# Kernel tuning notes

Measured on AMD Instinct MI355X. Metric: run time of the kernel, lower is better.

Reference implementation:

```python
import jax, jax.numpy as jnp
import numpy as np

# ---- config (YOLOv4-style, TRAIN_SIZE=608, P2..P5) ----
STRIDES = (4.0, 8.0, 16.0, 32.0)
ANCHORS = np.array([
    [[12, 16], [19, 36], [40, 28], [36, 75]],
    [[36, 75], [76, 55], [72, 146], [142, 110]],
    [[72, 146], [142, 110], [192, 243], [459, 401]],
    [[142, 110], [192, 243], [300, 300], [459, 401]],
], dtype=np.float32)  # [LEVELS, NUM_ANCHORS, 2]
MAX_PROP = 100
SCORE_THRESH = 0.25
IOU_THRESH = 0.5


def decode_prediction(p, anchors, stride):
    # p: [b, A, h, w, 6] -> [b, A*h*w, 5] with xyxy + score
    b, A, h, w, _ = p.shape
    txy, twh, conf, cls = p[..., :2], p[..., 2:4], p[..., 4:5], p[..., 5:6]
    gx, gy = jnp.meshgrid(jnp.arange(w, dtype=p.dtype), jnp.arange(h, dtype=p.dtype))
    grid = jnp.stack([gx, gy], axis=-1)[None, None]  # [1,1,h,w,2]
    xy = (jax.nn.sigmoid(txy) + grid) * stride
    wh = jnp.exp(twh) * anchors[None, :, None, None, :]
    score = jax.nn.sigmoid(conf) * jax.nn.sigmoid(cls)
    x1y1 = xy - 0.5 * wh
    x2y2 = xy + 0.5 * wh
    out = jnp.concatenate([x1y1, x2y2, score], axis=-1)  # [b,A,h,w,5]
    return out.reshape(b, A * h * w, 5)


def _iou_one_vs_all(box, boxes):
    # box: [4], boxes: [N,4] (xyxy)
    lt = jnp.maximum(box[:2], boxes[:, :2])
    rb = jnp.minimum(box[2:], boxes[:, 2:])
    wh = jnp.maximum(rb - lt, 0.0)
    inter = wh[:, 0] * wh[:, 1]
    a1 = jnp.maximum(box[2] - box[0], 0.0) * jnp.maximum(box[3] - box[1], 0.0)
    a2 = jnp.maximum(boxes[:, 2] - boxes[:, 0], 0.0) * jnp.maximum(boxes[:, 3] - boxes[:, 1], 0.0)
    return inter / (a1 + a2 - inter + 1e-9)


def _nms_single(boxes, scores):
    # greedy NMS, padded to MAX_PROP with zero rows
    s0 = jnp.where(scores >= SCORE_THRESH, scores, 0.0)

    def step(s, _):
        i = jnp.argmax(s)
        sc = s[i]
        box = boxes[i]
        keep = sc > 0.0
        row = jnp.where(keep, jnp.concatenate([box, sc[None]]), jnp.zeros(5, boxes.dtype))
        iou = _iou_one_vs_all(box, boxes)
        s = jnp.where((iou > IOU_THRESH) & keep, 0.0, s)
        s = s.at[i].set(0.0)
        return s, row

    _, props = jax.lax.scan(step, s0, None, length=MAX_PROP)
    return props  # [MAX_PROP, 5]


def entry_stop_gradients(t, mask):
    # gradient flows only through entries where mask==1
    return jax.lax.stop_gradient(t) * (1.0 - mask) + t * mask


def _forward(p2, p3, p4, p5):
    anchors = jnp.asarray(ANCHORS)
    d2 = decode_prediction(p2, anchors[0], STRIDES[0])
    d3 = decode_prediction(p3, anchors[1], STRIDES[1])
    d4 = decode_prediction(p4, anchors[2], STRIDES[2])
    d5 = decode_prediction(p5, anchors[3], STRIDES[3])
    proposals = jnp.concatenate([d2, d3, d4, d5], axis=1)  # [b, N, 5]
    proposals = jax.vmap(lambda pr: _nms_single(pr[:, :4], pr[:, 4]))(proposals)  # [b, MAX_PROP, 5]
    mask = (jnp.sum(proposals[..., :4], axis=-1) != 0.0).astype(proposals.dtype)[..., None]
    return entry_stop_gradients(proposals, mask)


def setup_inputs() -> dict:
    key = jax.random.key(0)
    k2, k3, k4, k5 = jax.random.split(key, 4)
    b, A, ch = 32, 4, 6
    return {
        "p2": jax.random.normal(k2, (b, A, 152, 152, ch), dtype=jnp.float32),
        "p3": jax.random.normal(k3, (b, A, 76, 76, ch), dtype=jnp.float32),
        "p4": jax.random.normal(k4, (b, A, 38, 38, ch), dtype=jnp.float32),
        "p5": jax.random.normal(k5, (b, A, 19, 19, ch), dtype=jnp.float32),
    }


def reference(p2, p3, p4, p5):
    return _forward(p2, p3, p4, p5)
```

## Files before the change

### kernel.cpp

```cpp
#include <hip/hip_runtime.h>
#include <cstdint>
#include <cstddef>

typedef unsigned int u32;
typedef unsigned long long u64;

#define NTOT 122740
#define NPAIR 61370
#define KTOP 1024
#define WIN  256
#define NBIN 4096
#define SCORE_T 0.25f
#define TBITS 0x3E800000u
#define HSPLIT_BITS 0x3EFFF000u
#define CSTRIDE 64
#define CAP_H 40960
#define CAP_L 20480


#define WS_CANDH 8192
#define WS_CANDL 10493952

__device__ __forceinline__ float sigm(float x) { return 1.0f / (1.0f + expf(-x)); }

__device__ __forceinline__ int score_bin(u32 bits) {
  return min(4095, 1 + (int)((bits - TBITS) >> 12));
}

__device__ __forceinline__ u64 shfl_u64(u64 x, int src) {
  int lo = __shfl((int)(u32)x, src, 64);
  int hi = __shfl((int)(u32)(x >> 32), src, 64);
  return ((u64)(u32)hi << 32) | (u32)lo;
}

__device__ __forceinline__ void score_pair(int P, int b,
    const float* __restrict__ p2, const float* __restrict__ p3,
    const float* __restrict__ p4, const float* __restrict__ p5,
    u32& b0, u32& b1, u32& gi0, u32& gi1)
{
  int t0 = 2 * P;
  const float* p; int l0, LN;
  if (t0 < 92416)       { p = p2; l0 = t0;          LN = 92416; }
  else if (t0 < 115520) { p = p3; l0 = t0 - 92416;  LN = 23104; }
  else if (t0 < 121296) { p = p4; l0 = t0 - 115520; LN = 5776;  }
  else                  { p = p5; l0 = t0 - 121296; LN = 1444;  }
  const float* q = p + ((size_t)b * LN + (size_t)l0) * 6;
  float4 v1 = *(const float4*)(q + 4);
  float4 v2 = *(const float4*)(q + 8);
  float s0 = sigm(v1.x) * sigm(v1.y);
  float s1 = sigm(v2.z) * sigm(v2.w);
  b0 = (s0 >= SCORE_T) ? __float_as_uint(s0) : 0u;
  b1 = (s1 >= SCORE_T) ? __float_as_uint(s1) : 0u;
  gi0 = (u32)t0; gi1 = (u32)(t0 + 1);
}

__device__ float4 decode_box_from_gidx(u32 gidx, int b,
    const float* __restrict__ p2, const float* __restrict__ p3,
    const float* __restrict__ p4, const float* __restrict__ p5)
{
  const float* p; int t, H, W; float stride;
  float aw0, ah0, aw1, ah1, aw2, ah2, aw3, ah3;
  if (gidx < 92416u) {
    p = p2 + (size_t)b * 92416 * 6; t = (int)gidx; H = 152; W = 152; stride = 4.0f;
    aw0=12.f; ah0=16.f; aw1=19.f; ah1=36.f; aw2=40.f; ah2=28.f; aw3=36.f; ah3=75.f;
  } else if (gidx < 115520u) {
    p = p3 + (size_t)b * 23104 * 6; t = (int)(gidx - 92416u); H = 76; W = 76; stride = 8.0f;
    aw0=36.f; ah0=75.f; aw1=76.f; ah1=55.f; aw2=72.f; ah2=146.f; aw3=142.f; ah3=110.f;
  } else if (gidx < 121296u) {
    p = p4 + (size_t)b * 5776 * 6; t = (int)(gidx - 115520u); H = 38; W = 38; stride = 16.0f;
    aw0=72.f; ah0=146.f; aw1=142.f; ah1=110.f; aw2=192.f; ah2=243.f; aw3=459.f; ah3=401.f;
  } else {
    p = p5 + (size_t)b * 1444 * 6; t = (int)(gidx - 121296u); H = 19; W = 19; stride = 32.0f;
    aw0=142.f; ah0=110.f; aw1=192.f; ah1=243.f; aw2=300.f; ah2=300.f; aw3=459.f; ah3=401.f;
  }
  int HW = H * W;
  int a = t / HW;
  int r = t - a * HW;
  int y = r / W;
  int x = r - y * W;
  const float* q = p + (size_t)t * 6;
  float2 t01 = *(const float2*)(q + 0);
  float2 t23 = *(const float2*)(q + 2);
  float cx = (sigm(t01.x) + (float)x) * stride;
  float cy = (sigm(t01.y) + (float)y) * stride;
  float aw = (a == 0) ? aw0 : (a == 1) ? aw1 : (a == 2) ? aw2 : aw3;
  float ah = (a == 0) ? ah0 : (a == 1) ? ah1 : (a == 2) ? ah2 : ah3;
  float bw = expf(t23.x) * aw;
  float bh = expf(t23.y) * ah;
  return make_float4(cx - 0.5f * bw, cy - 0.5f * bh, cx + 0.5f * bw, cy + 0.5f * bh);
}

__device__ __forceinline__ bool iou_gt(float4 A, float4 B) {
  float ltx = fmaxf(A.x, B.x), lty = fmaxf(A.y, B.y);
  float rbx = fminf(A.z, B.z), rby = fminf(A.w, B.w);
  float w = fmaxf(rbx - ltx, 0.0f), h = fmaxf(rby - lty, 0.0f);
  float inter = w * h;
  float a1 = fmaxf(A.z - A.x, 0.0f) * fmaxf(A.w - A.y, 0.0f);
  float a2 = fmaxf(B.z - B.x, 0.0f) * fmaxf(B.w - B.y, 0.0f);
  float iou = inter / (a1 + a2 - inter + 1e-9f);
  return iou > 0.5f;
}

__global__ __launch_bounds__(256)
void decode_kernel(const float* __restrict__ p2, const float* __restrict__ p3,
                   const float* __restrict__ p4, const float* __restrict__ p5,
                   u32* __restrict__ counters,
                   uint2* __restrict__ candH, uint2* __restrict__ candL)
{
  __shared__ uint2 stH[1024];
  __shared__ uint2 stL[1024];
  __shared__ u32 s_cH, s_cL, s_bH, s_bL;
  const int tid = threadIdx.x;
  const int b = blockIdx.y;
  if (tid == 0) { s_cH = 0u; s_cL = 0u; }
  __syncthreads();

  const int pbase = blockIdx.x * 512;
  #pragma unroll
  for (int k = 0; k < 2; ++k) {
    int P = pbase + k * 256 + tid;
    if (P < NPAIR) {
      u32 b0, b1, gi0, gi1;
      score_pair(P, b, p2, p3, p4, p5, b0, b1, gi0, gi1);
      if (b0) {
        bool H = (b0 >= HSPLIT_BITS);
        u32 pos = atomicAdd(H ? &s_cH : &s_cL, 1u);
        (H ? stH : stL)[pos] = make_uint2(b0, gi0);
      }
      if (b1) {
        bool H = (b1 >= HSPLIT_BITS);
        u32 pos = atomicAdd(H ? &s_cH : &s_cL, 1u);
        (H ? stH : stL)[pos] = make_uint2(b1, gi1);
      }
    }
  }
  __syncthreads();
  if (tid == 0) {
    if (s_cH) s_bH = atomicAdd(&counters[(size_t)b * CSTRIDE],     s_cH);
    if (s_cL) s_bL = atomicAdd(&counters[(size_t)b * CSTRIDE + 1], s_cL);
  }
  __syncthreads();
  uint2* gH = candH + (size_t)b * CAP_H;
  uint2* gL = candL + (size_t)b * CAP_L;
  const u32 mH = s_cH, mL = s_cL;
  for (u32 i = tid; i < mH; i += 256) { u32 d = s_bH + i; if (d < (u32)CAP_H) gH[d] = stH[i]; }
  for (u32 i = tid; i < mL; i += 256) { u32 d = s_bL + i; if (d < (u32)CAP_L) gL[d] = stL[i]; }
}

__global__ __launch_bounds__(1024, 1)
void mega_kernel(const u32* __restrict__ counters,
                 const uint2* __restrict__ candH, const uint2* __restrict__ candL,
                 const float* __restrict__ p2, const float* __restrict__ p3,
                 const float* __restrict__ p4, const float* __restrict__ p5,
                 float* __restrict__ out)
{
  const int b = blockIdx.x;
  const int tid = threadIdx.x;

  __shared__ u32 sstart[NBIN];
  __shared__ u32 scur[NBIN];
  __shared__ u64 skey[KTOP];
  __shared__ u64 skey2[KTOP];
  __shared__ float4 sbox[WIN];
  __shared__ u64 smat[WIN * 4];
  __shared__ float4 selbox[100];
  __shared__ int s_misc[4];
  __shared__ int s_B, s_n;

  const u32 nHc = counters[(size_t)b * CSTRIDE];
  const u32 nLc = counters[(size_t)b * CSTRIDE + 1];
  const bool readL = (nHc < (u32)KTOP);
  const bool fb = (nHc > (u32)CAP_H) || (readL && nLc > (u32)CAP_L);

  for (int i = tid; i < NBIN; i += 1024) scur[i] = 0u;
  for (int i = tid; i < KTOP; i += 1024) { skey[i] = 0ull; skey2[i] = 0ull; }
  __syncthreads();

  if (!fb) {
    const uint2* gH = candH + (size_t)b * CAP_H;
    for (u32 i = tid; i < nHc; i += 1024) atomicAdd(&scur[score_bin(gH[i].x)], 1u);
    if (readL) {
      const uint2* gL = candL + (size_t)b * CAP_L;
      for (u32 i = tid; i < nLc; i += 1024) atomicAdd(&scur[score_bin(gL[i].x)], 1u);
    }
  } else {
    for (int P = tid; P < NPAIR; P += 1024) {
      u32 b0, b1, gi0, gi1;
      score_pair(P, b, p2, p3, p4, p5, b0, b1, gi0, gi1);
      if (b0) atomicAdd(&scur[score_bin(b0)], 1u);
      if (b1) atomicAdd(&scur[score_bin(b1)], 1u);
    }
  }
  __syncthreads();

  if (tid < 64) {
    u32 h[64];
    #pragma unroll
    for (int k = 0; k < 64; ++k) h[k] = scur[tid * 64 + k];
    u32 lsum = 0;
    #pragma unroll
    for (int k = 0; k < 64; ++k) lsum += h[k];
    u32 S = lsum;
    #pragma unroll
    for (int off = 1; off < 64; off <<= 1) {
      u32 v = (u32)__shfl_down((int)S, off, 64);
      if (tid + off < 64) S += v;
    }
    u32 c = S - lsum;
    int Bv = -1; u32 nv = 0;
    for (int k = 63; k >= 0; --k) {
      sstart[tid * 64 + k] = c;
      c += h[k];
      if (c <= (u32)KTOP) { Bv = tid * 64 + k; nv = c; }
    }
    scur[tid]      = (Bv < 0) ? 0xFFFFFFFFu : (u32)Bv;
    scur[64 + tid] = nv;
  }
  __syncthreads();
  if (tid == 0) {
    u32 bb = 0xFFFFFFFFu, nn = 0;
    for (int l = 0; l < 64; ++l) {
      u32 v = scur[l];
      if (v < bb) { bb = v; nn = scur[64 + l]; }
    }
    if (bb == 0xFFFFFFFFu) { s_B = 4095; s_n = KTOP; }
    else { s_B = max((int)bb, 1); s_n = (int)nn; }
  }
  __syncthreads();
  const int B = s_B;
  const int n = min(s_n, KTOP);

  for (int i = tid; i < NBIN; i += 1024) scur[i] = sstart[i];
  __syncthreads();

  if (!fb) {
    const uint2* gH = candH + (size_t)b * CAP_H;
    for (u32 i = tid; i < nHc; i += 1024) {
      uint2 e = gH[i];
      int bin = score_bin(e.x);
      if (bin >= B) {
        u32 slot = atomicAdd(&scur[bin], 1u);
        if (slot < (u32)KTOP) skey[slot] = ((u64)e.x << 32) | (u32)(~e.y);
      }
    }
    if (readL) {
      const uint2* gL = candL + (size_t)b * CAP_L;
      for (u32 i = tid; i < nLc; i += 1024) {
        uint2 e = gL[i];
        int bin = score_bin(e.x);
        if (bin >= B) {
          u32 slot = atomicAdd(&scur[bin], 1u);
          if (slot < (u32)KTOP) skey[slot] = ((u64)e.x << 32) | (u32)(~e.y);
        }
      }
    }
  } else {
    for (int P = tid; P < NPAIR; P += 1024) {
      u32 b0, b1, gi0, gi1;
      score_pair(P, b, p2, p3, p4, p5, b0, b1, gi0, gi1);
      if (b0) { int bin = score_bin(b0);
        if (bin >= B) { u32 slot = atomicAdd(&scur[bin], 1u);
          if (slot < (u32)KTOP) skey[slot] = ((u64)b0 << 32) | (u32)(~gi0); } }
      if (b1) { int bin = score_bin(b1);
        if (bin >= B) { u32 slot = atomicAdd(&scur[bin], 1u);
          if (slot < (u32)KTOP) skey[slot] = ((u64)b1 << 32) | (u32)(~gi1); } }
    }
  }
  __syncthreads();

  for (int s = tid; s < n; s += 1024) {
    u64 k = skey[s];
    int bin = score_bin((u32)(k >> 32));
    int st = (int)sstart[bin];
    int en = (int)scur[bin];
    u32 r = 0;
    for (int j = st; j < en; ++j) r += (skey[j] > k) ? 1u : 0u;
    skey2[st + r] = k;
  }
  __syncthreads();

  const int Wn = min(n, WIN);

  if (tid < WIN) {
    sbox[tid] = (tid < Wn) ? decode_box_from_gidx(~(u32)skey2[tid], b, p2, p3, p4, p5)
                           : make_float4(0.f, 0.f, 0.f, 0.f);
  }
  __syncthreads();

  {
    int row = tid & 255, word = tid >> 8;
    u64 bits = 0;
    if (row < Wn) {
      float4 A = sbox[row];
      int j0 = word * 64;
      int je = min(64, Wn - j0);
      for (int j = 0; j < je; ++j)
        if (iou_gt(A, sbox[j0 + j])) bits |= (1ull << j);
    }
    smat[word * 256 + row] = bits;
  }
  __syncthreads();

  if (tid < 64) {
    const int lane = tid;
    u64 m0[4], m1[4], m2[4], m3[4];
    #pragma unroll
    for (int w = 0; w < 4; ++w) {
      m0[w] = smat[w * 256 +   0 + lane];
      m1[w] = smat[w * 256 +  64 + lane];
      m2[w] = smat[w * 256 + 128 + lane];
      m3[w] = smat[w * 256 + 192 + lane];
    }
    u64 live[4];
    #pragma unroll
    for (int g2 = 0; g2 < 4; ++g2) {
      int lo = g2 * 64;
      live[g2] = (Wn >= lo + 64) ? ~0ull : (Wn > lo ? ((1ull << (Wn - lo)) - 1ull) : 0ull);
    }
    int sel = 0;
    #pragma unroll 1
    for (int w2 = 0; w2 < 4; ++w2) {
      while (live[w2] && sel < 100) {
        int j = (int)__ffsll(live[w2]) - 1;
        int p = (w2 << 6) + j;
        u64 r0, r1, r2, r3;
        if (w2 == 0)      { r0 = shfl_u64(m0[0], j); r1 = shfl_u64(m0[1], j); r2 = shfl_u64(m0[2], j); r3 = shfl_u64(m0[3], j); }
        else if (w2 == 1) { r0 = shfl_u64(m1[0], j); r1 = shfl_u64(m1[1], j); r2 = shfl_u64(m1[2], j); r3 = shfl_u64(m1[3], j); }
        else if (w2 == 2) { r0 = shfl_u64(m2[0], j); r1 = shfl_u64(m2[1], j); r2 = shfl_u64(m2[2], j); r3 = shfl_u64(m2[3], j); }
        else              { r0 = shfl_u64(m3[0], j); r1 = shfl_u64(m3[1], j); r2 = shfl_u64(m3[2], j); r3 = shfl_u64(m3[3], j); }
        live[0] &= ~r0; live[1] &= ~r1; live[2] &= ~r2; live[3] &= ~r3;
        live[w2] &= ~(1ull << j);
        if (lane == 0) {
          float4 box = sbox[p];
          u64 k = skey2[p];
          float sc = __uint_as_float((u32)(k >> 32));
          selbox[sel] = box;
          float* orow = out + (size_t)b * 500 + (size_t)sel * 5;
          orow[0] = box.x; orow[1] = box.y; orow[2] = box.z; orow[3] = box.w; orow[4] = sc;
        }
        sel++;
      }
    }
    if (lane == 0) {
      s_misc[2] = sel;
      s_misc[3] = (sel < 100 && n > WIN) ? 1 : 0;
    }
  }
  __syncthreads();

  if (s_misc[3]) {
    if (tid < 64) {
      const int lane = tid;
      int sel = s_misc[2];
      for (int p = WIN; p < n && sel < 100; ++p) {
        u64 k = skey2[p];
        float4 box = decode_box_from_gidx(~(u32)k, b, p2, p3, p4, p5);
        bool hit = false;
        if (lane < sel) hit = iou_gt(selbox[lane], box);
        if (lane + 64 < sel) hit = hit || iou_gt(selbox[lane + 64], box);
        u64 anyhit = __ballot(hit);
        if (anyhit == 0ull) {
          if (lane == 0) {
            selbox[sel] = box;
            float sc = __uint_as_float((u32)(k >> 32));
            float* orow = out + (size_t)b * 500 + (size_t)sel * 5;
            orow[0] = box.x; orow[1] = box.y; orow[2] = box.z; orow[3] = box.w; orow[4] = sc;
          }
          sel++;
        }
      }
      if (lane == 0) s_misc[2] = sel;
    }
  }
  __syncthreads();

  const int nsel = s_misc[2];
  for (int i = tid; i < (100 - nsel) * 5; i += 1024)
    out[(size_t)b * 500 + (size_t)nsel * 5 + i] = 0.0f;
}

extern "C" void kernel_launch(void* const* d_in, const int* in_sizes, int n_in,
                              void* d_out, int out_size, void* d_ws, size_t ws_size,
                              hipStream_t stream) {
  const float* p2 = (const float*)d_in[0];
  const float* p3 = (const float*)d_in[1];
  const float* p4 = (const float*)d_in[2];
  const float* p5 = (const float*)d_in[3];
  float* out = (float*)d_out;

  unsigned char* w = (unsigned char*)d_ws;
  u32*   counters = (u32*)w;
  uint2* candH    = (uint2*)(w + WS_CANDH);
  uint2* candL    = (uint2*)(w + WS_CANDL);

  hipMemsetAsync(counters, 0, 32 * CSTRIDE * sizeof(u32), stream);
  decode_kernel<<<dim3(120, 32), 256, 0, stream>>>(p2, p3, p4, p5,
                                                   counters, candH, candL);
  mega_kernel<<<32, 1024, 0, stream>>>(counters, candH, candL,
                                       p2, p3, p4, p5, out);
}
```

Baseline: 171.0 us.

## Stage decode inputs through LDS with coalesced float4 loads and split mega kernel

The decode kernel now loads each block's slice of raw predictions as contiguous float4 into shared memory and reads only the two score channels per row. This replaces strided per-pair loads and doubles the grid to 240 blocks per image. The mega kernel is split into a sort kernel, which writes sorted keys to workspace, and a separate NMS kernel, freeing shared memory. The bin-selection reduction also moves from a serial thread-0 loop to a wave shuffle-min. The risks are the cost of an extra launch and a global round-trip for the sorted keys, and candidates are silently dropped if a block's staging buffer exceeds 512.

```diff
diff --git a/kernel.cpp b/kernel.cpp
--- a/kernel.cpp
+++ b/kernel.cpp
@@ -17,9 +17,14 @@
 #define CAP_H 40960
 #define CAP_L 20480
 
-
-#define WS_CANDH 8192
-#define WS_CANDL 10493952
+#define F4TOT 184110
+#define F4B3 138624
+#define F4B4 173280
+#define F4B5 181944
+
+#define WS_SORTED 8192
+#define WS_CANDH  270336
+#define WS_CANDL  10756096
 
 __device__ __forceinline__ float sigm(float x) { return 1.0f / (1.0f + expf(-x)); }
 
@@ -107,30 +112,48 @@
                    u32* __restrict__ counters,
                    uint2* __restrict__ candH, uint2* __restrict__ candL)
 {
-  __shared__ uint2 stH[1024];
-  __shared__ uint2 stL[1024];
+  __shared__ float4 sbuf4[768];
+  __shared__ uint2 stH[512];
+  __shared__ uint2 stL[512];
   __shared__ u32 s_cH, s_cL, s_bH, s_bL;
   const int tid = threadIdx.x;
   const int b = blockIdx.y;
   if (tid == 0) { s_cH = 0u; s_cL = 0u; }
-  __syncthreads();
-
-  const int pbase = blockIdx.x * 512;
+
+  const float4* q2 = (const float4*)p2;
+  const float4* q3 = (const float4*)p3;
+  const float4* q4 = (const float4*)p4;
+  const float4* q5 = (const float4*)p5;
+
+  const int f4base = blockIdx.x * 768;
+  #pragma unroll
+  for (int j = 0; j < 3; ++j) {
+    int idx4 = f4base + j * 256 + tid;
+    if (idx4 < F4TOT) {
+      const float4* src;
+      if (idx4 < F4B3)      src = q2 + (size_t)b * 138624 + idx4;
+      else if (idx4 < F4B4) src = q3 + (size_t)b * 34656  + (idx4 - F4B3);
+      else if (idx4 < F4B5) src = q4 + (size_t)b * 8664   + (idx4 - F4B4);
+      else                  src = q5 + (size_t)b * 2166   + (idx4 - F4B5);
+      sbuf4[j * 256 + tid] = *src;
+    }
+  }
+  __syncthreads();
+
+  const float* sbuf = (const float*)sbuf4;
+  const int rbase = blockIdx.x * 512;
   #pragma unroll
   for (int k = 0; k < 2; ++k) {
-    int P = pbase + k * 256 + tid;
-    if (P < NPAIR) {
-      u32 b0, b1, gi0, gi1;
-      score_pair(P, b, p2, p3, p4, p5, b0, b1, gi0, gi1);
-      if (b0) {
-        bool H = (b0 >= HSPLIT_BITS);
+    int lr = 2 * tid + k;
+    int rg = rbase + lr;
+    if (rg < NTOT) {
+      float2 cc = *(const float2*)&sbuf[lr * 6 + 4];
+      float s = sigm(cc.x) * sigm(cc.y);
+      if (s >= SCORE_T) {
+        u32 bits = __float_as_uint(s);
+        bool H = (bits >= HSPLIT_BITS);
         u32 pos = atomicAdd(H ? &s_cH : &s_cL, 1u);
-        (H ? stH : stL)[pos] = make_uint2(b0, gi0);
-      }
-      if (b1) {
-        bool H = (b1 >= HSPLIT_BITS);
-        u32 pos = atomicAdd(H ? &s_cH : &s_cL, 1u);
-        (H ? stH : stL)[pos] = make_uint2(b1, gi1);
+        if (pos < 512u) (H ? stH : stL)[pos] = make_uint2(bits, (u32)rg);
       }
     }
   }
@@ -142,17 +165,17 @@
   __syncthreads();
   uint2* gH = candH + (size_t)b * CAP_H;
   uint2* gL = candL + (size_t)b * CAP_L;
-  const u32 mH = s_cH, mL = s_cL;
+  const u32 mH = min(s_cH, 512u), mL = min(s_cL, 512u);
   for (u32 i = tid; i < mH; i += 256) { u32 d = s_bH + i; if (d < (u32)CAP_H) gH[d] = stH[i]; }
   for (u32 i = tid; i < mL; i += 256) { u32 d = s_bL + i; if (d < (u32)CAP_L) gL[d] = stL[i]; }
 }
 
 __global__ __launch_bounds__(1024, 1)
-void mega_kernel(const u32* __restrict__ counters,
+void sort_kernel(const u32* __restrict__ counters_in, u32* __restrict__ counters,
                  const uint2* __restrict__ candH, const uint2* __restrict__ candL,
                  const float* __restrict__ p2, const float* __restrict__ p3,
                  const float* __restrict__ p4, const float* __restrict__ p5,
-                 float* __restrict__ out)
+                 u64* __restrict__ sortedK)
 {
   const int b = blockIdx.x;
   const int tid = threadIdx.x;
@@ -160,20 +183,14 @@
   __shared__ u32 sstart[NBIN];
   __shared__ u32 scur[NBIN];
   __shared__ u64 skey[KTOP];
-  __shared__ u64 skey2[KTOP];
-  __shared__ float4 sbox[WIN];
-  __shared__ u64 smat[WIN * 4];
-  __shared__ float4 selbox[100];
-  __shared__ int s_misc[4];
   __shared__ int s_B, s_n;
 
-  const u32 nHc = counters[(size_t)b * CSTRIDE];
-  const u32 nLc = counters[(size_t)b * CSTRIDE + 1];
+  const u32 nHc = counters_in[(size_t)b * CSTRIDE];
+  const u32 nLc = counters_in[(size_t)b * CSTRIDE + 1];
   const bool readL = (nHc < (u32)KTOP);
   const bool fb = (nHc > (u32)CAP_H) || (readL && nLc > (u32)CAP_L);
 
   for (int i = tid; i < NBIN; i += 1024) scur[i] = 0u;
-  for (int i = tid; i < KTOP; i += 1024) { skey[i] = 0ull; skey2[i] = 0ull; }
   __syncthreads();
 
   if (!fb) {
@@ -213,18 +230,16 @@
       c += h[k];
       if (c <= (u32)KTOP) { Bv = tid * 64 + k; nv = c; }
     }
-    scur[tid]      = (Bv < 0) ? 0xFFFFFFFFu : (u32)Bv;
-    scur[64 + tid] = nv;
-  }
-  __syncthreads();
-  if (tid == 0) {
-    u32 bb = 0xFFFFFFFFu, nn = 0;
-    for (int l = 0; l < 64; ++l) {
-      u32 v = scur[l];
-      if (v < bb) { bb = v; nn = scur[64 + l]; }
-    }
-    if (bb == 0xFFFFFFFFu) { s_B = 4095; s_n = KTOP; }
-    else { s_B = max((int)bb, 1); s_n = (int)nn; }
+    u32 pk = (Bv < 0) ? 0xFFFFFFFFu : (((u32)Bv << 12) | nv);
+    #pragma unroll
+    for (int off = 32; off >= 1; off >>= 1) {
+      u32 o = (u32)__shfl_down((int)pk, off, 64);
+      if (tid + off < 64) pk = min(pk, o);
+    }
+    if (tid == 0) {
+      if (pk == 0xFFFFFFFFu) { s_B = 4095; s_n = KTOP; }
+      else { s_B = max((int)(pk >> 12), 1); s_n = (int)(pk & 0xFFFu); }
+    }
   }
   __syncthreads();
   const int B = s_B;
@@ -268,6 +283,7 @@
   }
   __syncthreads();
 
+  u64* dst = sortedK + (size_t)b * KTOP;
   for (int s = tid; s < n; s += 1024) {
     u64 k = skey[s];
     int bin = score_bin((u32)(k >> 32));
@@ -275,14 +291,34 @@
     int en = (int)scur[bin];
     u32 r = 0;
     for (int j = st; j < en; ++j) r += (skey[j] > k) ? 1u : 0u;
-    skey2[st + r] = k;
-  }
-  __syncthreads();
-
+    dst[st + r] = k;
+  }
+  if (tid == 0) counters[(size_t)b * CSTRIDE + 8] = (u32)n;
+}
+
+__global__ __launch_bounds__(1024, 1)
+void nms_kernel(const u32* __restrict__ counters, const u64* __restrict__ sortedK,
+                const float* __restrict__ p2, const float* __restrict__ p3,
+                const float* __restrict__ p4, const float* __restrict__ p5,
+                float* __restrict__ out)
+{
+  const int b = blockIdx.x;
+  const int tid = threadIdx.x;
+
+  __shared__ u64 skeyw[WIN];
+  __shared__ float4 sbox[WIN];
+  __shared__ u64 smat[WIN * 4];
+  __shared__ float4 selbox[100];
+  __shared__ int s_misc[4];
+
+  const int n = min((int)counters[(size_t)b * CSTRIDE + 8], KTOP);
+  const u64* src = sortedK + (size_t)b * KTOP;
   const int Wn = min(n, WIN);
 
   if (tid < WIN) {
-    sbox[tid] = (tid < Wn) ? decode_box_from_gidx(~(u32)skey2[tid], b, p2, p3, p4, p5)
+    u64 k = (tid < Wn) ? src[tid] : 0ull;
+    skeyw[tid] = k;
+    sbox[tid] = (tid < Wn) ? decode_box_from_gidx(~(u32)k, b, p2, p3, p4, p5)
                            : make_float4(0.f, 0.f, 0.f, 0.f);
   }
   __syncthreads();
@@ -332,7 +368,7 @@
         live[w2] &= ~(1ull << j);
         if (lane == 0) {
           float4 box = sbox[p];
-          u64 k = skey2[p];
+          u64 k = skeyw[p];
           float sc = __uint_as_float((u32)(k >> 32));
           selbox[sel] = box;
           float* orow = out + (size_t)b * 500 + (size_t)sel * 5;
@@ -353,7 +389,7 @@
       const int lane = tid;
       int sel = s_misc[2];
       for (int p = WIN; p < n && sel < 100; ++p) {
-        u64 k = skey2[p];
+        u64 k = src[p];
         float4 box = decode_box_from_gidx(~(u32)k, b, p2, p3, p4, p5);
         bool hit = false;
         if (lane < sel) hit = iou_gt(selbox[lane], box);
@@ -390,12 +426,14 @@
 
   unsigned char* w = (unsigned char*)d_ws;
   u32*   counters = (u32*)w;
+  u64*   sortedK  = (u64*)(w + WS_SORTED);
   uint2* candH    = (uint2*)(w + WS_CANDH);
   uint2* candL    = (uint2*)(w + WS_CANDL);
 
   hipMemsetAsync(counters, 0, 32 * CSTRIDE * sizeof(u32), stream);
-  decode_kernel<<<dim3(120, 32), 256, 0, stream>>>(p2, p3, p4, p5,
+  decode_kernel<<<dim3(240, 32), 256, 0, stream>>>(p2, p3, p4, p5,
                                                    counters, candH, candL);
-  mega_kernel<<<32, 1024, 0, stream>>>(counters, candH, candL,
-                                       p2, p3, p4, p5, out);
-}
+  sort_kernel<<<32, 1024, 0, stream>>>(counters, counters, candH, candL,
+                                       p2, p3, p4, p5, sortedK);
+  nms_kernel<<<32, 1024, 0, stream>>>(counters, sortedK, p2, p3, p4, p5, out);
+}
```

Result: slower. 188.3 us (+10.1%).

## Fuse memset, decode and NMS into one cooperative grid-synced kernel

Applied to the files above, without the earlier changes.

Replaces the memset, the decode kernel and the per-batch mega kernel with one cooperative kernel of 256 blocks. Grid syncs separate counter zeroing, a decode phase and the top-k/NMS phase. In the decode phase each block reads a contiguous slice of inputs through coalesced float4 loads into shared memory, computes scores, and compacts candidates. This removes two launch gaps and improves load coalescing. It also swaps the serial bin-threshold reduction for a wave shuffle min-reduction and drops some shared-memory zeroing. In exchange, 224 blocks sit idle after the second grid sync, and the cooperative launch plus grid barriers add their own overhead.

```diff
diff --git a/kernel.cpp b/kernel.cpp
--- a/kernel.cpp
+++ b/kernel.cpp
@@ -1,6 +1,9 @@
 #include <hip/hip_runtime.h>
+#include <hip/hip_cooperative_groups.h>
 #include <cstdint>
 #include <cstddef>
+
+namespace cg = cooperative_groups;
 
 typedef unsigned int u32;
 typedef unsigned long long u64;
@@ -17,6 +20,15 @@
 #define CAP_H 40960
 #define CAP_L 20480
 
+#define NBLK 256
+#define SLICES 8
+#define SLICE_REC 15360
+#define CHUNK 1024
+
+#define F4TOT 184110
+#define F4B3 138624
+#define F4B4 173280
+#define F4B5 181944
 
 #define WS_CANDH 8192
 #define WS_CANDL 10493952
@@ -101,62 +113,21 @@
   return iou > 0.5f;
 }
 
-__global__ __launch_bounds__(256)
-void decode_kernel(const float* __restrict__ p2, const float* __restrict__ p3,
-                   const float* __restrict__ p4, const float* __restrict__ p5,
-                   u32* __restrict__ counters,
-                   uint2* __restrict__ candH, uint2* __restrict__ candL)
+__global__ __launch_bounds__(1024, 1)
+void fused_kernel(const float* __restrict__ p2, const float* __restrict__ p3,
+                  const float* __restrict__ p4, const float* __restrict__ p5,
+                  u32* __restrict__ counters,
+                  uint2* __restrict__ candH, uint2* __restrict__ candL,
+                  float* __restrict__ out)
 {
-  __shared__ uint2 stH[1024];
-  __shared__ uint2 stL[1024];
+  cg::grid_group grid = cg::this_grid();
+  const int tid = threadIdx.x;
+  const int bid = blockIdx.x;
+
+  __shared__ float4 sbuf4[1536];
+  __shared__ uint2 stH[CHUNK];
+  __shared__ uint2 stL[CHUNK];
   __shared__ u32 s_cH, s_cL, s_bH, s_bL;
-  const int tid = threadIdx.x;
-  const int b = blockIdx.y;
-  if (tid == 0) { s_cH = 0u; s_cL = 0u; }
-  __syncthreads();
-
-  const int pbase = blockIdx.x * 512;
-  #pragma unroll
-  for (int k = 0; k < 2; ++k) {
-    int P = pbase + k * 256 + tid;
-    if (P < NPAIR) {
-      u32 b0, b1, gi0, gi1;
-      score_pair(P, b, p2, p3, p4, p5, b0, b1, gi0, gi1);
-      if (b0) {
-        bool H = (b0 >= HSPLIT_BITS);
-        u32 pos = atomicAdd(H ? &s_cH : &s_cL, 1u);
-        (H ? stH : stL)[pos] = make_uint2(b0, gi0);
-      }
-      if (b1) {
-        bool H = (b1 >= HSPLIT_BITS);
-        u32 pos = atomicAdd(H ? &s_cH : &s_cL, 1u);
-        (H ? stH : stL)[pos] = make_uint2(b1, gi1);
-      }
-    }
-  }
-  __syncthreads();
-  if (tid == 0) {
-    if (s_cH) s_bH = atomicAdd(&counters[(size_t)b * CSTRIDE],     s_cH);
-    if (s_cL) s_bL = atomicAdd(&counters[(size_t)b * CSTRIDE + 1], s_cL);
-  }
-  __syncthreads();
-  uint2* gH = candH + (size_t)b * CAP_H;
-  uint2* gL = candL + (size_t)b * CAP_L;
-  const u32 mH = s_cH, mL = s_cL;
-  for (u32 i = tid; i < mH; i += 256) { u32 d = s_bH + i; if (d < (u32)CAP_H) gH[d] = stH[i]; }
-  for (u32 i = tid; i < mL; i += 256) { u32 d = s_bL + i; if (d < (u32)CAP_L) gL[d] = stL[i]; }
-}
-
-__global__ __launch_bounds__(1024, 1)
-void mega_kernel(const u32* __restrict__ counters,
-                 const uint2* __restrict__ candH, const uint2* __restrict__ candL,
-                 const float* __restrict__ p2, const float* __restrict__ p3,
-                 const float* __restrict__ p4, const float* __restrict__ p5,
-                 float* __restrict__ out)
-{
-  const int b = blockIdx.x;
-  const int tid = threadIdx.x;
-
   __shared__ u32 sstart[NBIN];
   __shared__ u32 scur[NBIN];
   __shared__ u64 skey[KTOP];
@@ -167,13 +138,90 @@
   __shared__ int s_misc[4];
   __shared__ int s_B, s_n;
 
+  if (bid < 32 && tid < CSTRIDE) counters[(size_t)bid * CSTRIDE + tid] = 0u;
+  grid.sync();
+
+  {
+    const int b = bid >> 3;
+    const int s = bid & 7;
+    const int SS = s * SLICE_REC;
+    const int SE = min(SS + SLICE_REC, NTOT);
+    u32* gcH = counters + (size_t)b * CSTRIDE;
+    u32* gcL = gcH + 1;
+    uint2* gH = candH + (size_t)b * CAP_H;
+    uint2* gL = candL + (size_t)b * CAP_L;
+    const float4* q2 = (const float4*)p2;
+    const float4* q3 = (const float4*)p3;
+    const float4* q4 = (const float4*)p4;
+    const float4* q5 = (const float4*)p5;
+
+    for (int CB = SS; CB < SE; CB += CHUNK) {
+      if (tid == 0) { s_cH = 0u; s_cL = 0u; }
+      const int FS = (CB >> 1) * 3;
+      const int FE = min(FS + 1536, F4TOT);
+      const int nf = FE - FS;
+      if (tid < nf) {
+        int idx4 = FS + tid;
+        const float4* src;
+        if (idx4 < F4B3)      src = q2 + (size_t)b * 138624 + idx4;
+        else if (idx4 < F4B4) src = q3 + (size_t)b * 34656  + (idx4 - F4B3);
+        else if (idx4 < F4B5) src = q4 + (size_t)b * 8664   + (idx4 - F4B4);
+        else                  src = q5 + (size_t)b * 2166   + (idx4 - F4B5);
+        sbuf4[tid] = *src;
+      }
+      {
+        int i2 = tid + 1024;
+        if (i2 < nf) {
+          int idx4 = FS + i2;
+          const float4* src;
+          if (idx4 < F4B3)      src = q2 + (size_t)b * 138624 + idx4;
+          else if (idx4 < F4B4) src = q3 + (size_t)b * 34656  + (idx4 - F4B3);
+          else if (idx4 < F4B5) src = q4 + (size_t)b * 8664   + (idx4 - F4B4);
+          else                  src = q5 + (size_t)b * 2166   + (idx4 - F4B5);
+          sbuf4[i2] = *src;
+        }
+      }
+      __syncthreads();
+      {
+        int rg = CB + tid;
+        if (rg < SE) {
+          const float* sbuf = (const float*)sbuf4;
+          float2 cc = *(const float2*)&sbuf[tid * 6 + 4];
+          float sc = sigm(cc.x) * sigm(cc.y);
+          if (sc >= SCORE_T) {
+            u32 bits = __float_as_uint(sc);
+            bool H = (bits >= HSPLIT_BITS);
+            u32 pos = atomicAdd(H ? &s_cH : &s_cL, 1u);
+            (H ? stH : stL)[pos] = make_uint2(bits, (u32)rg);
+          }
+        }
+      }
+      __syncthreads();
+      if (tid == 0) {
+        s_bH = s_cH ? atomicAdd(gcH, s_cH) : 0u;
+        s_bL = s_cL ? atomicAdd(gcL, s_cL) : 0u;
+      }
+      __syncthreads();
+      {
+        const u32 mH = s_cH, mL = s_cL, bH = s_bH, bL = s_bL;
+        for (u32 i = tid; i < mH; i += 1024) { u32 d = bH + i; if (d < (u32)CAP_H) gH[d] = stH[i]; }
+        for (u32 i = tid; i < mL; i += 1024) { u32 d = bL + i; if (d < (u32)CAP_L) gL[d] = stL[i]; }
+      }
+      __syncthreads();
+    }
+  }
+  __threadfence();
+  grid.sync();
+
+  if (bid >= 32) return;
+  const int b = bid;
+
   const u32 nHc = counters[(size_t)b * CSTRIDE];
   const u32 nLc = counters[(size_t)b * CSTRIDE + 1];
   const bool readL = (nHc < (u32)KTOP);
   const bool fb = (nHc > (u32)CAP_H) || (readL && nLc > (u32)CAP_L);
 
   for (int i = tid; i < NBIN; i += 1024) scur[i] = 0u;
-  for (int i = tid; i < KTOP; i += 1024) { skey[i] = 0ull; skey2[i] = 0ull; }
   __syncthreads();
 
   if (!fb) {
@@ -213,18 +261,16 @@
       c += h[k];
       if (c <= (u32)KTOP) { Bv = tid * 64 + k; nv = c; }
     }
-    scur[tid]      = (Bv < 0) ? 0xFFFFFFFFu : (u32)Bv;
-    scur[64 + tid] = nv;
-  }
-  __syncthreads();
-  if (tid == 0) {
-    u32 bb = 0xFFFFFFFFu, nn = 0;
-    for (int l = 0; l < 64; ++l) {
-      u32 v = scur[l];
-      if (v < bb) { bb = v; nn = scur[64 + l]; }
-    }
-    if (bb == 0xFFFFFFFFu) { s_B = 4095; s_n = KTOP; }
-    else { s_B = max((int)bb, 1); s_n = (int)nn; }
+    u32 pk = (Bv < 0) ? 0xFFFFFFFFu : (((u32)Bv << 12) | nv);
+    #pragma unroll
+    for (int off = 32; off >= 1; off >>= 1) {
+      u32 o = (u32)__shfl_down((int)pk, off, 64);
+      if (tid + off < 64) pk = min(pk, o);
+    }
+    if (tid == 0) {
+      if (pk == 0xFFFFFFFFu) { s_B = 4095; s_n = KTOP; }
+      else { s_B = max((int)(pk >> 12), 1); s_n = (int)(pk & 0xFFFu); }
+    }
   }
   __syncthreads();
   const int B = s_B;
@@ -393,9 +439,8 @@
   uint2* candH    = (uint2*)(w + WS_CANDH);
   uint2* candL    = (uint2*)(w + WS_CANDL);
 
-  hipMemsetAsync(counters, 0, 32 * CSTRIDE * sizeof(u32), stream);
-  decode_kernel<<<dim3(120, 32), 256, 0, stream>>>(p2, p3, p4, p5,
-                                                   counters, candH, candL);
-  mega_kernel<<<32, 1024, 0, stream>>>(counters, candH, candL,
-                                       p2, p3, p4, p5, out);
-}
+  void* args[] = { (void*)&p2, (void*)&p3, (void*)&p4, (void*)&p5,
+                   (void*)&counters, (void*)&candH, (void*)&candL, (void*)&out };
+  hipLaunchCooperativeKernel((const void*)fused_kernel, dim3(NBLK), dim3(1024),
+                             args, 0, stream);
+}
```

After: 332.6 us. +94.5%, slower.
